# Kernel optimization log

Measured on AMD Instinct MI355X. Metric: run time of the kernel, lower is better.

The kernel has to match this reference:

```python
import jax, jax.numpy as jnp
import numpy as np

N_NODES = 100000


def setup_inputs() -> dict:
    key = jax.random.key(0)
    k1, k2, k3 = jax.random.split(key, 3)
    x = jax.random.normal(k1, (N_NODES, 128), dtype=jnp.float32)
    edge_index = jax.random.randint(k2, (2, 1600000), 0, N_NODES, dtype=jnp.int32)
    # GCNConv linear weight: [out_features, in_features], bias: [out_features]
    W = jax.random.normal(k3, (128, 128), dtype=jnp.float32) * (1.0 / np.sqrt(128.0))
    b = jnp.zeros((128,), dtype=jnp.float32)
    return {"x": x, "edge_index": edge_index, "W": W, "b": b}


def reference(x, edge_index, W, b):
    n = x.shape[0]
    # --- add self loops (PyG GCNConv default) ---
    loop = jnp.arange(n, dtype=edge_index.dtype)
    row = jnp.concatenate([edge_index[0], loop])  # source nodes
    col = jnp.concatenate([edge_index[1], loop])  # target nodes
    # --- symmetric degree normalization D^{-1/2} A_hat D^{-1/2} ---
    ones = jnp.ones(row.shape[0], dtype=x.dtype)
    deg = jax.ops.segment_sum(ones, col, num_segments=n)
    deg_inv_sqrt = jnp.where(deg > 0, jax.lax.rsqrt(deg), 0.0)
    norm = deg_inv_sqrt[row] * deg_inv_sqrt[col]  # [E + N]
    # --- linear transform then gather-normalize-scatter aggregation ---
    xw = x @ W.T  # [N, out]
    msgs = xw[row] * norm[:, None]  # [E + N, out]
    out = jax.ops.segment_sum(msgs, col, num_segments=n)  # [N, out]
    return out + b
```

## Files before the change

kernel.cpp:

```cpp
#include <hip/hip_runtime.h>

#define NF 128
#define WLD2 136

#define BSHIFT 9
#define BNODES (1 << BSHIFT)
#define NBUCK 196
#define BCAP 10240
#define CHUNK 4096

typedef __attribute__((ext_vector_type(8))) short bf16x8;
typedef __attribute__((ext_vector_type(4))) float f32x4;

__device__ inline short f2bf_rne(float f) {
    unsigned u = __float_as_uint(f);
    u += 0x7FFFu + ((u >> 16) & 1u);
    return (short)(u >> 16);
}

__global__ void binit_kernel(int* __restrict__ bcursor) {
    int i = blockIdx.x * blockDim.x + threadIdx.x;
    if (i < NBUCK) bcursor[i] = i * BCAP;
}

__global__ __launch_bounds__(256) void bucketize_kernel(const int* __restrict__ row,
                                                        const int* __restrict__ col,
                                                        int* __restrict__ bcursor,
                                                        int2* __restrict__ bpairs, int E) {
    __shared__ int2 pe[CHUNK];
    __shared__ int hist[NBUCK];
    __shared__ int base[NBUCK];
    const int t = threadIdx.x;
    const int e0 = blockIdx.x * CHUNK;
    const int cnt = min(CHUNK, E - e0);
    for (int i = t; i < NBUCK; i += 256) hist[i] = 0;
    __syncthreads();
    for (int i = t; i < cnt; i += 256) {
        int c = col[e0 + i];
        int r = row[e0 + i];
        pe[i] = make_int2(c, r);
        atomicAdd(&hist[c >> BSHIFT], 1);
    }
    __syncthreads();
    for (int i = t; i < NBUCK; i += 256) {
        int h = hist[i];
        base[i] = h ? atomicAdd(&bcursor[i], h) : 0;
        hist[i] = 0;
    }
    __syncthreads();
    for (int i = t; i < cnt; i += 256) {
        int2 p = pe[i];
        int bk = p.x >> BSHIFT;
        int pos = base[bk] + atomicAdd(&hist[bk], 1);
        bpairs[pos] = p;
    }
}

__global__ __launch_bounds__(256) void bcount_kernel(const int2* __restrict__ bpairs,
                                                     const int* __restrict__ bcursor,
                                                     int* __restrict__ cnt,
                                                     float* __restrict__ dis, int N) {
    __shared__ int h[BNODES];
    const int b = blockIdx.x;
    const int node0 = b << BSHIFT;
    const int nn = min(BNODES, N - node0);
    for (int i = threadIdx.x; i < nn; i += 256) h[i] = 0;
    __syncthreads();
    const int start = b * BCAP;
    const int end = bcursor[b];
    for (int i = start + threadIdx.x; i < end; i += 256)
        atomicAdd(&h[bpairs[i].x - node0], 1);
    __syncthreads();
    for (int i = threadIdx.x; i < nn; i += 256) {
        int c = h[i];
        cnt[node0 + i] = c;
        dis[node0 + i] = rsqrtf((float)c + 1.0f);
    }
}

__device__ inline int block_exclusive_scan_256(int val) {
    __shared__ int wsum[4];
    int lane = threadIdx.x & 63, wave = threadIdx.x >> 6;
    int x = val;
#pragma unroll
    for (int off = 1; off < 64; off <<= 1) {
        int y = __shfl_up(x, off, 64);
        if (lane >= off) x += y;
    }
    if (lane == 63) wsum[wave] = x;
    __syncthreads();
    if (threadIdx.x == 0) {
        int acc = 0;
        for (int w = 0; w < 4; ++w) { int t = wsum[w]; wsum[w] = acc; acc += t; }
    }
    __syncthreads();
    return x - val + wsum[wave];
}

__global__ __launch_bounds__(256) void scan_partials(const int* __restrict__ cnt,
                                                     int* __restrict__ bsum, int n) {
    __shared__ int lds[4];
    int base = blockIdx.x * 1024;
    int s = 0;
    for (int i = threadIdx.x; i < 1024; i += 256) {
        int idx = base + i;
        if (idx < n) s += cnt[idx];
    }
#pragma unroll
    for (int off = 32; off > 0; off >>= 1) s += __shfl_down(s, off, 64);
    int lane = threadIdx.x & 63, wave = threadIdx.x >> 6;
    if (lane == 0) lds[wave] = s;
    __syncthreads();
    if (threadIdx.x == 0) bsum[blockIdx.x] = lds[0] + lds[1] + lds[2] + lds[3];
}

__global__ __launch_bounds__(256) void scan_bsums(int* __restrict__ bsum, int B) {
    int t = threadIdx.x;
    int v = (t < B) ? bsum[t] : 0;
    int exc = block_exclusive_scan_256(v);
    if (t < B) bsum[t] = exc;
}

__global__ __launch_bounds__(256) void scan_final(const int* __restrict__ cnt,
                                                  const int* __restrict__ bsum,
                                                  int* __restrict__ offs, int n) {
    int base = blockIdx.x * 1024 + threadIdx.x * 4;
    int v0 = 0, v1 = 0, v2 = 0, v3 = 0;
    if (base + 3 < n) {
        int4 v = *(const int4*)(cnt + base);
        v0 = v.x; v1 = v.y; v2 = v.z; v3 = v.w;
    } else {
        if (base + 0 < n) v0 = cnt[base + 0];
        if (base + 1 < n) v1 = cnt[base + 1];
        if (base + 2 < n) v2 = cnt[base + 2];
        if (base + 3 < n) v3 = cnt[base + 3];
    }
    int s = v0 + v1 + v2 + v3;
    int exc = block_exclusive_scan_256(s) + bsum[blockIdx.x];
    int o0 = exc, o1 = o0 + v0, o2 = o1 + v1, o3 = o2 + v2;
    if (base + 3 < n) {
        *(int4*)(offs + base) = make_int4(o0, o1, o2, o3);
    } else {
        if (base + 0 < n) offs[base + 0] = o0;
        if (base + 1 < n) offs[base + 1] = o1;
        if (base + 2 < n) offs[base + 2] = o2;
        if (base + 3 < n) offs[base + 3] = o3;
    }
}

__global__ __launch_bounds__(256) void csr_fill_kernel(const int2* __restrict__ bpairs,
                                                       const int* __restrict__ bcursor,
                                                       const int* __restrict__ offs,
                                                       int* __restrict__ ed, int N) {
    __shared__ int cur[BNODES];
    const int b = blockIdx.x;
    const int node0 = b << BSHIFT;
    const int nn = min(BNODES, N - node0);
    for (int i = threadIdx.x; i < nn; i += 256) cur[i] = offs[node0 + i];
    __syncthreads();
    const int start = b * BCAP;
    const int end = bcursor[b];
    for (int i = start + threadIdx.x; i < end; i += 256) {
        int2 p = bpairs[i];
        int pos = atomicAdd(&cur[p.x - node0], 1);
        ed[pos] = p.y;
    }
}

__global__ __launch_bounds__(256) void gemm_xws_kernel(const float* __restrict__ x,
                                                       const float* __restrict__ W,
                                                       const float* __restrict__ dis,
                                                       unsigned short* __restrict__ xws,
                                                       int n) {
    __shared__ short Wl[NF * WLD2];

    for (int idx = threadIdx.x; idx < NF * 32; idx += 256) {
        int o = idx >> 5;
        int kq = (idx & 31) << 2;
        float4 v = *(const float4*)(W + o * NF + kq);
        short* d = &Wl[o * WLD2 + kq];
        d[0] = f2bf_rne(v.x); d[1] = f2bf_rne(v.y);
        d[2] = f2bf_rne(v.z); d[3] = f2bf_rne(v.w);
    }
    __syncthreads();

    const int lane = threadIdx.x & 63;
    const int wave = threadIdx.x >> 6;
    const int mbase = wave * 32;
    const int l15 = lane & 15;
    const int quad = lane >> 4;
    const int tile = blockIdx.x * 128;

    f32x4 acc[2][8];
#pragma unroll
    for (int mb = 0; mb < 2; ++mb)
#pragma unroll
        for (int nb = 0; nb < 8; ++nb) acc[mb][nb] = (f32x4)0.0f;

#pragma unroll
    for (int kc = 0; kc < 4; ++kc) {
        const int kof = kc * 32 + quad * 8;
        bf16x8 Bf[8];
#pragma unroll
        for (int nb = 0; nb < 8; ++nb) {
            int o = nb * 16 + l15;
            Bf[nb] = *(const bf16x8*)(&Wl[o * WLD2 + kof]);
        }
#pragma unroll
        for (int mb = 0; mb < 2; ++mb) {
            int r = tile + mbase + mb * 16 + l15;
            if (r >= n) r = n - 1;
            const float4* ap = (const float4*)(x + (size_t)r * NF + kof);
            float4 a0 = ap[0], a1 = ap[1];
            bf16x8 Af;
            Af[0] = f2bf_rne(a0.x); Af[1] = f2bf_rne(a0.y);
            Af[2] = f2bf_rne(a0.z); Af[3] = f2bf_rne(a0.w);
            Af[4] = f2bf_rne(a1.x); Af[5] = f2bf_rne(a1.y);
            Af[6] = f2bf_rne(a1.z); Af[7] = f2bf_rne(a1.w);
#pragma unroll
            for (int nb = 0; nb < 8; ++nb)
                acc[mb][nb] = __builtin_amdgcn_mfma_f32_16x16x32_bf16(Af, Bf[nb], acc[mb][nb], 0, 0, 0);
        }
    }

#pragma unroll
    for (int mb = 0; mb < 2; ++mb) {
        int rbase = tile + mbase + mb * 16 + quad * 4;
#pragma unroll
        for (int reg = 0; reg < 4; ++reg) {
            int r = rbase + reg;
            if (r < n) {
                float dsc = dis[r];
#pragma unroll
                for (int nb = 0; nb < 8; ++nb) {
                    int c = nb * 16 + l15;
                    xws[(size_t)r * NF + c] = (unsigned short)f2bf_rne(acc[mb][nb][reg] * dsc);
                }
            }
        }
    }
}

__global__ __launch_bounds__(256) void gather_kernel(const int* __restrict__ ed,
                                                     const int* __restrict__ offs,
                                                     const int* __restrict__ cnt,
                                                     const float* __restrict__ dis,
                                                     const unsigned* __restrict__ xws,
                                                     const float* __restrict__ b,
                                                     float* __restrict__ out, int n) {
    int node = (int)((blockIdx.x * blockDim.x + threadIdx.x) >> 6);
    int lane = threadIdx.x & 63;
    if (node >= n) return;
    float dc = dis[node];
    int start = offs[node];
    int end = start + cnt[node];
    float ax = 0.f, ay = 0.f;
    int i = start;
    for (; i + 4 <= end; i += 4) {
        int s0 = ed[i], s1 = ed[i + 1], s2 = ed[i + 2], s3 = ed[i + 3];
        unsigned u0 = xws[(size_t)s0 * 64 + lane];
        unsigned u1 = xws[(size_t)s1 * 64 + lane];
        unsigned u2 = xws[(size_t)s2 * 64 + lane];
        unsigned u3 = xws[(size_t)s3 * 64 + lane];
        ax += __uint_as_float(u0 << 16) + __uint_as_float(u1 << 16) +
              __uint_as_float(u2 << 16) + __uint_as_float(u3 << 16);
        ay += __uint_as_float(u0 & 0xFFFF0000u) + __uint_as_float(u1 & 0xFFFF0000u) +
              __uint_as_float(u2 & 0xFFFF0000u) + __uint_as_float(u3 & 0xFFFF0000u);
    }
    for (; i < end; ++i) {
        unsigned u = xws[(size_t)ed[i] * 64 + lane];
        ax += __uint_as_float(u << 16);
        ay += __uint_as_float(u & 0xFFFF0000u);
    }
    unsigned us = xws[(size_t)node * 64 + lane];
    ax += __uint_as_float(us << 16);
    ay += __uint_as_float(us & 0xFFFF0000u);
    float2 bb = ((const float2*)b)[lane];
    float2 o;
    o.x = fmaf(ax, dc, bb.x);
    o.y = fmaf(ay, dc, bb.y);
    ((float2*)(out + (size_t)node * NF))[lane] = o;
}

extern "C" void kernel_launch(void* const* d_in, const int* in_sizes, int n_in,
                              void* d_out, int out_size, void* d_ws, size_t ws_size,
                              hipStream_t stream) {
    const float* x = (const float*)d_in[0];
    const int* ei = (const int*)d_in[1];
    const float* W = (const float*)d_in[2];
    const float* b = (const float*)d_in[3];
    float* out = (float*)d_out;

    const int N = in_sizes[0] / NF;
    const int E = in_sizes[1] / 2;
    const int* row = ei;
    const int* col = ei + E;

    char* ws = (char*)d_ws;
    unsigned short* xws = (unsigned short*)ws;
    ws += (size_t)N * NF * sizeof(unsigned short);
    int* cnt = (int*)ws; ws += (size_t)N * sizeof(int);
    float* dis = (float*)ws; ws += (size_t)N * sizeof(float);
    int* offs = (int*)ws; ws += (size_t)N * sizeof(int);
    int2* bpairs = (int2*)ws; ws += (size_t)NBUCK * BCAP * sizeof(int2);
    int* bcursor = (int*)ws; ws += 256 * sizeof(int);
    int* ed = (int*)ws; ws += (size_t)E * sizeof(int);
    int* bsum = (int*)ws;

    const int B = (N + 1023) / 1024;
    const int CB = (E + CHUNK - 1) / CHUNK;

    binit_kernel<<<1, 256, 0, stream>>>(bcursor);
    bucketize_kernel<<<CB, 256, 0, stream>>>(row, col, bcursor, bpairs, E);

    bcount_kernel<<<NBUCK, 256, 0, stream>>>(bpairs, bcursor, cnt, dis, N);

    scan_partials<<<B, 256, 0, stream>>>(cnt, bsum, N);
    scan_bsums<<<1, 256, 0, stream>>>(bsum, B);
    scan_final<<<B, 256, 0, stream>>>(cnt, bsum, offs, N);

    gemm_xws_kernel<<<(N + 127) / 128, 256, 0, stream>>>(x, W, dis, xws, N);

    csr_fill_kernel<<<NBUCK, 256, 0, stream>>>(bpairs, bcursor, offs, ed, N);

    {
        int nodes_per_block = 256 / 64;
        int blocks = (N + nodes_per_block - 1) / nodes_per_block;
        gather_kernel<<<blocks, 256, 0, stream>>>(ed, offs, cnt, dis,
                                                  (const unsigned*)xws, b, out, N);
    }
}
```

Before: 251.6 us.

## Fuse degree count, scan and CSR fill into one bucket kernel; half-wave gather

Replaces the count, three-pass global scan and CSR fill kernels with one per-bucket kernel. It caches the bucket's edge pairs in LDS (80KB), builds a local histogram, scans it, and writes offsets relative to the bucket's fixed region. This drops four launches and a second global read of bpairs. The gather kernel now has each half-wave load a different neighbor row with 8-byte loads and combines the halves with a cross-lane shuffle, so each wave handles two edges per load. Risks are the large LDS footprint per block, which limits occupancy, and CSR offsets that now carry gaps between buckets.

```diff
diff --git a/kernel.cpp b/kernel.cpp
--- a/kernel.cpp
+++ b/kernel.cpp
@@ -17,6 +17,8 @@
     u += 0x7FFFu + ((u >> 16) & 1u);
     return (short)(u >> 16);
 }
+__device__ inline float bf_lo(unsigned u) { return __uint_as_float(u << 16); }
+__device__ inline float bf_hi(unsigned u) { return __uint_as_float(u & 0xFFFF0000u); }
 
 __global__ void binit_kernel(int* __restrict__ bcursor) {
     int i = blockIdx.x * blockDim.x + threadIdx.x;
@@ -56,114 +58,68 @@
     }
 }
 
-__global__ __launch_bounds__(256) void bcount_kernel(const int2* __restrict__ bpairs,
-                                                     const int* __restrict__ bcursor,
-                                                     int* __restrict__ cnt,
-                                                     float* __restrict__ dis, int N) {
+__device__ inline int block_exclusive_scan_256(int val) {
+    __shared__ int wsum[4];
+    int lane = threadIdx.x & 63, wave = threadIdx.x >> 6;
+    int x = val;
+#pragma unroll
+    for (int off = 1; off < 64; off <<= 1) {
+        int y = __shfl_up(x, off, 64);
+        if (lane >= off) x += y;
+    }
+    if (lane == 63) wsum[wave] = x;
+    __syncthreads();
+    if (threadIdx.x == 0) {
+        int acc = 0;
+        for (int w = 0; w < 4; ++w) { int t = wsum[w]; wsum[w] = acc; acc += t; }
+    }
+    __syncthreads();
+    return x - val + wsum[wave];
+}
+
+__global__ __launch_bounds__(256) void bucket_build_kernel(const int2* __restrict__ bpairs,
+                                                           const int* __restrict__ bcursor,
+                                                           int* __restrict__ cnt,
+                                                           float* __restrict__ dis,
+                                                           int* __restrict__ offs,
+                                                           int* __restrict__ ed, int N) {
+    __shared__ int2 pe[BCAP];
     __shared__ int h[BNODES];
     const int b = blockIdx.x;
     const int node0 = b << BSHIFT;
     const int nn = min(BNODES, N - node0);
+    const int start = b * BCAP;
+    const int ecnt = bcursor[b] - start;
     for (int i = threadIdx.x; i < nn; i += 256) h[i] = 0;
     __syncthreads();
-    const int start = b * BCAP;
-    const int end = bcursor[b];
-    for (int i = start + threadIdx.x; i < end; i += 256)
-        atomicAdd(&h[bpairs[i].x - node0], 1);
-    __syncthreads();
-    for (int i = threadIdx.x; i < nn; i += 256) {
-        int c = h[i];
-        cnt[node0 + i] = c;
-        dis[node0 + i] = rsqrtf((float)c + 1.0f);
-    }
-}
-
-__device__ inline int block_exclusive_scan_256(int val) {
-    __shared__ int wsum[4];
-    int lane = threadIdx.x & 63, wave = threadIdx.x >> 6;
-    int x = val;
-#pragma unroll
-    for (int off = 1; off < 64; off <<= 1) {
-        int y = __shfl_up(x, off, 64);
-        if (lane >= off) x += y;
-    }
-    if (lane == 63) wsum[wave] = x;
-    __syncthreads();
-    if (threadIdx.x == 0) {
-        int acc = 0;
-        for (int w = 0; w < 4; ++w) { int t = wsum[w]; wsum[w] = acc; acc += t; }
-    }
-    __syncthreads();
-    return x - val + wsum[wave];
-}
-
-__global__ __launch_bounds__(256) void scan_partials(const int* __restrict__ cnt,
-                                                     int* __restrict__ bsum, int n) {
-    __shared__ int lds[4];
-    int base = blockIdx.x * 1024;
-    int s = 0;
-    for (int i = threadIdx.x; i < 1024; i += 256) {
-        int idx = base + i;
-        if (idx < n) s += cnt[idx];
-    }
-#pragma unroll
-    for (int off = 32; off > 0; off >>= 1) s += __shfl_down(s, off, 64);
-    int lane = threadIdx.x & 63, wave = threadIdx.x >> 6;
-    if (lane == 0) lds[wave] = s;
-    __syncthreads();
-    if (threadIdx.x == 0) bsum[blockIdx.x] = lds[0] + lds[1] + lds[2] + lds[3];
-}
-
-__global__ __launch_bounds__(256) void scan_bsums(int* __restrict__ bsum, int B) {
-    int t = threadIdx.x;
-    int v = (t < B) ? bsum[t] : 0;
-    int exc = block_exclusive_scan_256(v);
-    if (t < B) bsum[t] = exc;
-}
-
-__global__ __launch_bounds__(256) void scan_final(const int* __restrict__ cnt,
-                                                  const int* __restrict__ bsum,
-                                                  int* __restrict__ offs, int n) {
-    int base = blockIdx.x * 1024 + threadIdx.x * 4;
-    int v0 = 0, v1 = 0, v2 = 0, v3 = 0;
-    if (base + 3 < n) {
-        int4 v = *(const int4*)(cnt + base);
-        v0 = v.x; v1 = v.y; v2 = v.z; v3 = v.w;
-    } else {
-        if (base + 0 < n) v0 = cnt[base + 0];
-        if (base + 1 < n) v1 = cnt[base + 1];
-        if (base + 2 < n) v2 = cnt[base + 2];
-        if (base + 3 < n) v3 = cnt[base + 3];
-    }
-    int s = v0 + v1 + v2 + v3;
-    int exc = block_exclusive_scan_256(s) + bsum[blockIdx.x];
-    int o0 = exc, o1 = o0 + v0, o2 = o1 + v1, o3 = o2 + v2;
-    if (base + 3 < n) {
-        *(int4*)(offs + base) = make_int4(o0, o1, o2, o3);
-    } else {
-        if (base + 0 < n) offs[base + 0] = o0;
-        if (base + 1 < n) offs[base + 1] = o1;
-        if (base + 2 < n) offs[base + 2] = o2;
-        if (base + 3 < n) offs[base + 3] = o3;
-    }
-}
-
-__global__ __launch_bounds__(256) void csr_fill_kernel(const int2* __restrict__ bpairs,
-                                                       const int* __restrict__ bcursor,
-                                                       const int* __restrict__ offs,
-                                                       int* __restrict__ ed, int N) {
-    __shared__ int cur[BNODES];
-    const int b = blockIdx.x;
-    const int node0 = b << BSHIFT;
-    const int nn = min(BNODES, N - node0);
-    for (int i = threadIdx.x; i < nn; i += 256) cur[i] = offs[node0 + i];
-    __syncthreads();
-    const int start = b * BCAP;
-    const int end = bcursor[b];
-    for (int i = start + threadIdx.x; i < end; i += 256) {
-        int2 p = bpairs[i];
-        int pos = atomicAdd(&cur[p.x - node0], 1);
-        ed[pos] = p.y;
+    for (int i = threadIdx.x; i < ecnt; i += 256) {
+        int2 p = bpairs[start + i];
+        p.x -= node0;
+        pe[i] = p;
+        atomicAdd(&h[p.x], 1);
+    }
+    __syncthreads();
+    const int t = threadIdx.x;
+    int v0 = (2 * t < nn) ? h[2 * t] : 0;
+    int v1 = (2 * t + 1 < nn) ? h[2 * t + 1] : 0;
+    int exc = block_exclusive_scan_256(v0 + v1);
+    if (2 * t < nn) {
+        offs[node0 + 2 * t] = start + exc;
+        cnt[node0 + 2 * t] = v0;
+        dis[node0 + 2 * t] = rsqrtf((float)v0 + 1.0f);
+        h[2 * t] = exc;
+    }
+    if (2 * t + 1 < nn) {
+        offs[node0 + 2 * t + 1] = start + exc + v0;
+        cnt[node0 + 2 * t + 1] = v1;
+        dis[node0 + 2 * t + 1] = rsqrtf((float)v1 + 1.0f);
+        h[2 * t + 1] = exc + v0;
+    }
+    __syncthreads();
+    for (int i = threadIdx.x; i < ecnt; i += 256) {
+        int2 p = pe[i];
+        int pos = atomicAdd(&h[p.x], 1);
+        ed[start + pos] = p.y;
     }
 }
 
@@ -245,41 +201,62 @@
                                                      const int* __restrict__ offs,
                                                      const int* __restrict__ cnt,
                                                      const float* __restrict__ dis,
-                                                     const unsigned* __restrict__ xws,
+                                                     const unsigned short* __restrict__ xws,
                                                      const float* __restrict__ b,
                                                      float* __restrict__ out, int n) {
     int node = (int)((blockIdx.x * blockDim.x + threadIdx.x) >> 6);
-    int lane = threadIdx.x & 63;
+    const int lane = threadIdx.x & 63;
     if (node >= n) return;
-    float dc = dis[node];
-    int start = offs[node];
-    int end = start + cnt[node];
-    float ax = 0.f, ay = 0.f;
+    node = __builtin_amdgcn_readfirstlane(node);
+    const int lsub = lane & 31;
+    const bool lo = lane < 32;
+    const float dc = dis[node];
+    const int start = offs[node];
+    const int end = start + cnt[node];
+
+    float ax = 0.f, ay = 0.f, az = 0.f, aw = 0.f;
+    {
+        uint2 u = *(const uint2*)(xws + (size_t)node * NF + lsub * 4);
+        if (lo) { ax = bf_lo(u.x); ay = bf_hi(u.x); az = bf_lo(u.y); aw = bf_hi(u.y); }
+    }
     int i = start;
-    for (; i + 4 <= end; i += 4) {
-        int s0 = ed[i], s1 = ed[i + 1], s2 = ed[i + 2], s3 = ed[i + 3];
-        unsigned u0 = xws[(size_t)s0 * 64 + lane];
-        unsigned u1 = xws[(size_t)s1 * 64 + lane];
-        unsigned u2 = xws[(size_t)s2 * 64 + lane];
-        unsigned u3 = xws[(size_t)s3 * 64 + lane];
-        ax += __uint_as_float(u0 << 16) + __uint_as_float(u1 << 16) +
-              __uint_as_float(u2 << 16) + __uint_as_float(u3 << 16);
-        ay += __uint_as_float(u0 & 0xFFFF0000u) + __uint_as_float(u1 & 0xFFFF0000u) +
-              __uint_as_float(u2 & 0xFFFF0000u) + __uint_as_float(u3 & 0xFFFF0000u);
-    }
-    for (; i < end; ++i) {
-        unsigned u = xws[(size_t)ed[i] * 64 + lane];
-        ax += __uint_as_float(u << 16);
-        ay += __uint_as_float(u & 0xFFFF0000u);
-    }
-    unsigned us = xws[(size_t)node * 64 + lane];
-    ax += __uint_as_float(us << 16);
-    ay += __uint_as_float(us & 0xFFFF0000u);
-    float2 bb = ((const float2*)b)[lane];
-    float2 o;
-    o.x = fmaf(ax, dc, bb.x);
-    o.y = fmaf(ay, dc, bb.y);
-    ((float2*)(out + (size_t)node * NF))[lane] = o;
+    for (; i + 8 <= end; i += 8) {
+        int r0 = ed[i], r1 = ed[i + 1], r2 = ed[i + 2], r3 = ed[i + 3];
+        int r4 = ed[i + 4], r5 = ed[i + 5], r6 = ed[i + 6], r7 = ed[i + 7];
+        int sa = lo ? r0 : r1, sb = lo ? r2 : r3, sc = lo ? r4 : r5, sd = lo ? r6 : r7;
+        uint2 ua = *(const uint2*)(xws + (size_t)sa * NF + lsub * 4);
+        uint2 ub = *(const uint2*)(xws + (size_t)sb * NF + lsub * 4);
+        uint2 uc = *(const uint2*)(xws + (size_t)sc * NF + lsub * 4);
+        uint2 ud = *(const uint2*)(xws + (size_t)sd * NF + lsub * 4);
+        ax += bf_lo(ua.x) + bf_lo(ub.x) + bf_lo(uc.x) + bf_lo(ud.x);
+        ay += bf_hi(ua.x) + bf_hi(ub.x) + bf_hi(uc.x) + bf_hi(ud.x);
+        az += bf_lo(ua.y) + bf_lo(ub.y) + bf_lo(uc.y) + bf_lo(ud.y);
+        aw += bf_hi(ua.y) + bf_hi(ub.y) + bf_hi(uc.y) + bf_hi(ud.y);
+    }
+    for (; i + 2 <= end; i += 2) {
+        int r0 = ed[i], r1 = ed[i + 1];
+        int s = lo ? r0 : r1;
+        uint2 u = *(const uint2*)(xws + (size_t)s * NF + lsub * 4);
+        ax += bf_lo(u.x); ay += bf_hi(u.x); az += bf_lo(u.y); aw += bf_hi(u.y);
+    }
+    if (i < end) {
+        int r0 = ed[i];
+        uint2 u = *(const uint2*)(xws + (size_t)r0 * NF + lsub * 4);
+        if (lo) { ax += bf_lo(u.x); ay += bf_hi(u.x); az += bf_lo(u.y); aw += bf_hi(u.y); }
+    }
+    ax += __shfl_xor(ax, 32, 64);
+    ay += __shfl_xor(ay, 32, 64);
+    az += __shfl_xor(az, 32, 64);
+    aw += __shfl_xor(aw, 32, 64);
+    if (lo) {
+        float4 bb = ((const float4*)b)[lsub];
+        float4 o;
+        o.x = fmaf(ax, dc, bb.x);
+        o.y = fmaf(ay, dc, bb.y);
+        o.z = fmaf(az, dc, bb.z);
+        o.w = fmaf(aw, dc, bb.w);
+        ((float4*)(out + (size_t)node * NF))[lsub] = o;
+    }
 }
 
 extern "C" void kernel_launch(void* const* d_in, const int* in_sizes, int n_in,
@@ -304,29 +281,20 @@
     int* offs = (int*)ws; ws += (size_t)N * sizeof(int);
     int2* bpairs = (int2*)ws; ws += (size_t)NBUCK * BCAP * sizeof(int2);
     int* bcursor = (int*)ws; ws += 256 * sizeof(int);
-    int* ed = (int*)ws; ws += (size_t)E * sizeof(int);
-    int* bsum = (int*)ws;
-
-    const int B = (N + 1023) / 1024;
+    int* ed = (int*)ws;
+
     const int CB = (E + CHUNK - 1) / CHUNK;
 
     binit_kernel<<<1, 256, 0, stream>>>(bcursor);
     bucketize_kernel<<<CB, 256, 0, stream>>>(row, col, bcursor, bpairs, E);
 
-    bcount_kernel<<<NBUCK, 256, 0, stream>>>(bpairs, bcursor, cnt, dis, N);
-
-    scan_partials<<<B, 256, 0, stream>>>(cnt, bsum, N);
-    scan_bsums<<<1, 256, 0, stream>>>(bsum, B);
-    scan_final<<<B, 256, 0, stream>>>(cnt, bsum, offs, N);
+    bucket_build_kernel<<<NBUCK, 256, 0, stream>>>(bpairs, bcursor, cnt, dis, offs, ed, N);
 
     gemm_xws_kernel<<<(N + 127) / 128, 256, 0, stream>>>(x, W, dis, xws, N);
-
-    csr_fill_kernel<<<NBUCK, 256, 0, stream>>>(bpairs, bcursor, offs, ed, N);
 
     {
         int nodes_per_block = 256 / 64;
         int blocks = (N + nodes_per_block - 1) / nodes_per_block;
-        gather_kernel<<<blocks, 256, 0, stream>>>(ed, offs, cnt, dis,
-                                                  (const unsigned*)xws, b, out, N);
-    }
-}
+        gather_kernel<<<blocks, 256, 0, stream>>>(ed, offs, cnt, dis, xws, b, out, N);
+    }
+}
```

After: 226.9 us. 1.11x faster.
